# Kernel tuning notes

Measured on AMD Instinct MI355X. Metric: run time of the kernel, lower is better.

The kernel has to match this reference:

```python
import jax, jax.numpy as jnp
import numpy as np

H = 4        # no_heads
CH = 32      # per-head hidden (c_hidden)
INF = 1.0e9

def setup_inputs() -> dict:
    key = jax.random.key(0)
    ks = jax.random.split(key, 8)
    B, I, J, C = 1, 256, 256, 128
    s = 0.02
    return {
        "x": jax.random.normal(ks[0], (B, I, J, C), jnp.float32),
        "mask": jnp.ones((B, I, J), jnp.float32),
        "chunk_size": 0,
        "ln_w": jnp.ones((C,), jnp.float32),
        "ln_b": jnp.zeros((C,), jnp.float32),
        "w_tri": jax.random.normal(ks[1], (C, H), jnp.float32) * s,
        "wq": jax.random.normal(ks[2], (C, H * CH), jnp.float32) * s,
        "wk": jax.random.normal(ks[3], (C, H * CH), jnp.float32) * s,
        "wv": jax.random.normal(ks[4], (C, H * CH), jnp.float32) * s,
        "wg": jax.random.normal(ks[5], (C, H * CH), jnp.float32) * s,
        "bg": jnp.zeros((H * CH,), jnp.float32),
        "wo": jax.random.normal(ks[6], (H * CH, C), jnp.float32) * s,
        "bo": jnp.zeros((C,), jnp.float32),
    }

def _layer_norm(x, w, b, eps=1e-5):
    mu = jnp.mean(x, axis=-1, keepdims=True)
    var = jnp.mean(jnp.square(x - mu), axis=-1, keepdims=True)
    return (x - mu) * jax.lax.rsqrt(var + eps) * w + b

def reference(x, mask, chunk_size, ln_w, ln_b, w_tri, wq, wk, wv, wg, bg, wo, bo):
    # starting=True -> no transpose of (I, J)
    B, I, J, C = x.shape
    xn = _layer_norm(x, ln_w, ln_b)                                   # [B,I,J,C]
    # biases
    mask_bias = (INF * (mask - 1.0))[:, :, None, None, :]             # [B,I,1,1,J]
    tri_bias = jnp.einsum("bijc,ch->bhij", xn, w_tri)[:, None]        # [B,1,H,I,J]
    # gated multi-head attention over the J axis (per row I)
    q = (xn @ wq).reshape(B, I, J, H, CH) * (CH ** -0.5)              # [B,I,J,H,CH]
    k = (xn @ wk).reshape(B, I, J, H, CH)
    v = (xn @ wv).reshape(B, I, J, H, CH)
    scores = jnp.einsum("biqhd,bikhd->bihqk", q, k) + mask_bias + tri_bias
    a = jax.nn.softmax(scores, axis=-1)                               # [B,I,H,J,J]
    o = jnp.einsum("bihqk,bikhd->biqhd", a, v)                        # [B,I,J,H,CH]
    g = jax.nn.sigmoid(xn @ wg + bg).reshape(B, I, J, H, CH)
    o = (o * g).reshape(B, I, J, H * CH)
    return o @ wo + bo                                                # [B,I,J,C]
```

## Files before the change

### kernel.cpp

```cpp
#include <hip/hip_runtime.h>
#include <math.h>

#define NI 256
#define NJ 256
#define NC 128
#define NH 4
#define NCH 32

typedef __attribute__((ext_vector_type(8)))  __bf16        bf16x8;
typedef __attribute__((ext_vector_type(8)))  unsigned short u16x8;
typedef __attribute__((ext_vector_type(4)))  unsigned int   u32x4;
typedef __attribute__((ext_vector_type(16))) float         f32x16;

__device__ __forceinline__ unsigned short f2bf(float f) {
    unsigned u = __builtin_bit_cast(unsigned, f);
    u += 0x7fffu + ((u >> 16) & 1u);
    return (unsigned short)(u >> 16);
}
__device__ __forceinline__ float bf2f(unsigned short s) {
    return __builtin_bit_cast(float, ((unsigned)s) << 16);
}
__device__ __forceinline__ f32x16 fzero16() {
    f32x16 z;
#pragma unroll
    for (int r = 0; r < 16; ++r) z[r] = 0.f;
    return z;
}
__device__ __forceinline__ f32x16 mfma16(bf16x8 a, bf16x8 b, f32x16 c) {
    return __builtin_amdgcn_mfma_f32_32x32x16_bf16(a, b, c, 0, 0, 0);
}

__global__ __launch_bounds__(256) void convert_weights(
    const float* __restrict__ wq, const float* __restrict__ wk,
    const float* __restrict__ wv, const float* __restrict__ wg,
    const float* __restrict__ wo, const float* __restrict__ w_tri,
    unsigned short* __restrict__ Wt_all, unsigned short* __restrict__ Wto,
    unsigned short* __restrict__ Wtri_pad)
{
    int id = blockIdx.x * 256 + threadIdx.x;
    if (id < 4 * 16384) {
        int m = id >> 14, r = id & 16383;
        int kk = r >> 7, c = r & 127;
        const float* W = (m == 0) ? wq : (m == 1) ? wk : (m == 2) ? wv : wg;
        Wt_all[(m * 128 + c) * 128 + kk] = f2bf(W[kk * 128 + c]);
    } else if (id < 5 * 16384) {
        int r = id - 4 * 16384;
        int kk = r >> 7, c = r & 127;
        Wto[c * 128 + kk] = f2bf(wo[kk * 128 + c]);
    } else {
        int r = id - 5 * 16384;
        int col = r >> 7, kk = r & 127;
        Wtri_pad[col * 128 + kk] = (col < NH) ? f2bf(w_tri[kk * NH + col]) : (unsigned short)0;
    }
}

#define XNP 136
__global__ __launch_bounds__(256, 2) void ln_proj_mfma(
    const float* __restrict__ x, const float* __restrict__ ln_w, const float* __restrict__ ln_b,
    const unsigned short* __restrict__ Wt_all, const unsigned short* __restrict__ Wtri_pad,
    const float* __restrict__ bg,
    unsigned short* __restrict__ q, unsigned short* __restrict__ k,
    unsigned short* __restrict__ v, unsigned short* __restrict__ g,
    float* __restrict__ tri)
{
    __shared__ unsigned short xn[64 * XNP];
    const int tid = threadIdx.x;
    const long tok0 = (long)blockIdx.x * 64;

    const int lane8 = tid & 7;
#pragma unroll
    for (int p = 0; p < 2; ++p) {
        const int t = p * 32 + (tid >> 3);
        const float4* xrow = (const float4*)(x + (tok0 + t) * NC + lane8 * 16);
        float4 xv[4];
        float s = 0.f;
#pragma unroll
        for (int u = 0; u < 4; ++u) {
            xv[u] = xrow[u];
            s += xv[u].x + xv[u].y + xv[u].z + xv[u].w;
        }
#pragma unroll
        for (int off = 4; off; off >>= 1) s += __shfl_down(s, off, 8);
        const float mu = __shfl(s, 0, 8) * (1.f / (float)NC);
        float s2 = 0.f;
#pragma unroll
        for (int u = 0; u < 4; ++u) {
            float dx;
            dx = xv[u].x - mu; s2 += dx * dx;
            dx = xv[u].y - mu; s2 += dx * dx;
            dx = xv[u].z - mu; s2 += dx * dx;
            dx = xv[u].w - mu; s2 += dx * dx;
        }
#pragma unroll
        for (int off = 4; off; off >>= 1) s2 += __shfl_down(s2, off, 8);
        const float rstd = rsqrtf(__shfl(s2, 0, 8) * (1.f / (float)NC) + 1e-5f);
#pragma unroll
        for (int u = 0; u < 4; ++u) {
            const int c = lane8 * 16 + u * 4;
            const float4 lw = *(const float4*)(ln_w + c);
            const float4 lb = *(const float4*)(ln_b + c);
            float o0 = (xv[u].x - mu) * rstd * lw.x + lb.x;
            float o1 = (xv[u].y - mu) * rstd * lw.y + lb.y;
            float o2 = (xv[u].z - mu) * rstd * lw.z + lb.z;
            float o3 = (xv[u].w - mu) * rstd * lw.w + lb.w;
            unsigned p0 = (unsigned)f2bf(o0) | ((unsigned)f2bf(o1) << 16);
            unsigned p1 = (unsigned)f2bf(o2) | ((unsigned)f2bf(o3) << 16);
            *(unsigned*)&xn[t * XNP + c]     = p0;
            *(unsigned*)&xn[t * XNP + c + 2] = p1;
        }
    }
    __syncthreads();

    const int w = tid >> 6, L = tid & 63, lh = L >> 5, lc = L & 31;
    f32x16 acc[2][4], accT[2];
#pragma unroll
    for (int mt = 0; mt < 2; ++mt) {
        accT[mt] = fzero16();
#pragma unroll
        for (int nt = 0; nt < 4; ++nt) acc[mt][nt] = fzero16();
    }

#pragma unroll
    for (int k0 = 0; k0 < 8; ++k0) {
        bf16x8 a0 = *(const bf16x8*)&xn[(lc)      * XNP + k0 * 16 + lh * 8];
        bf16x8 a1 = *(const bf16x8*)&xn[(32 + lc) * XNP + k0 * 16 + lh * 8];
#pragma unroll
        for (int nt = 0; nt < 4; ++nt) {
            const int ntile = w + 4 * nt;
            bf16x8 b = *(const bf16x8*)&Wt_all[(ntile * 32 + lc) * 128 + k0 * 16 + lh * 8];
            acc[0][nt] = mfma16(a0, b, acc[0][nt]);
            acc[1][nt] = mfma16(a1, b, acc[1][nt]);
        }
        bf16x8 bt = *(const bf16x8*)&Wtri_pad[lc * 128 + k0 * 16 + lh * 8];
        accT[0] = mfma16(a0, bt, accT[0]);
        accT[1] = mfma16(a1, bt, accT[1]);
    }

    const int a_row = (int)(tok0 >> 8);
    const int b0    = (int)(tok0 & 255);
    int rowl[16];
#pragma unroll
    for (int r = 0; r < 16; ++r) rowl[r] = (r & 3) + 8 * (r >> 2) + 4 * lh;

    const float bgv = bg[w * 32 + lc];
#pragma unroll
    for (int nt = 0; nt < 4; ++nt) {
        unsigned short* O = (nt == 0) ? q : (nt == 1) ? k : (nt == 2) ? v : g;
        unsigned short* Ob = O + (((long)a_row * NH + w) * NJ + b0) * NCH + lc;
#pragma unroll
        for (int mt = 0; mt < 2; ++mt) {
#pragma unroll
            for (int r = 0; r < 16; ++r) {
                const int row = mt * 32 + rowl[r];
                float val = acc[mt][nt][r];
                if (nt == 0) val *= 0.17677669529663689f;
                if (nt == 3) val = __builtin_amdgcn_rcpf(1.f + __expf(-(val + bgv)));
                Ob[(long)row * NCH] = f2bf(val);
            }
        }
    }
    if (lc < NH) {
        float* tb = tri + ((long)lc * NI + a_row) * NJ + b0;
#pragma unroll
        for (int mt = 0; mt < 2; ++mt)
#pragma unroll
            for (int r = 0; r < 16; ++r)
                tb[mt * 32 + rowl[r]] = accT[mt][r];
    }
}

#define LSP 260
__global__ __launch_bounds__(256) void swizzle_triT(
    const float* __restrict__ tri, float* __restrict__ tswz)
{
    __shared__ float Ls[32 * LSP];
    const int h = blockIdx.x, qt = blockIdx.y;
    const int tid = threadIdx.x;
#pragma unroll
    for (int it = 0; it < 8; ++it) {
        const int fi = it * 256 + tid;
        const int row = fi >> 6, c4 = fi & 63;
        *(float4*)&Ls[row * LSP + c4 * 4] =
            *(const float4*)(tri + ((long)h * NI + qt * 32 + row) * NJ + c4 * 4);
    }
    __syncthreads();
    const int kt = tid >> 5;
    const int lane2 = (tid & 31) * 2;
    float* dst = tswz + (((long)(h * 8 + qt) * 8 + kt) * 64 + lane2) * 16;
#pragma unroll
    for (int sub = 0; sub < 2; ++sub) {
        const int lane = lane2 + sub;
        const int lc = lane & 31, lhh = lane >> 5;
        float vals[16];
#pragma unroll
        for (int r = 0; r < 16; ++r)
            vals[r] = Ls[lc * LSP + kt * 32 + (r & 3) + 8 * (r >> 2) + 4 * lhh];
#pragma unroll
        for (int u = 0; u < 4; ++u)
            *(float4*)(dst + sub * 16 + u * 4) =
                make_float4(vals[4*u], vals[4*u+1], vals[4*u+2], vals[4*u+3]);
    }
}

#define KSP 40
#define VTP 264
#define GSP 40
#define OSP 36
__global__ __launch_bounds__(256, 2) void attn_fused(
    const unsigned short* __restrict__ q, const unsigned short* __restrict__ k,
    const unsigned short* __restrict__ v, const unsigned short* __restrict__ g,
    const float* __restrict__ tswz, const float* __restrict__ mask,
    const unsigned short* __restrict__ Wto, const float* __restrict__ bo,
    float* __restrict__ out)
{
    __shared__ char smem[48640];
    unsigned short* Ks = (unsigned short*)smem;
    unsigned short* Vt = (unsigned short*)(smem + 20480);
    unsigned short* Gs = (unsigned short*)(smem + 37376);
    float*       maskb = (float*)(smem + 47616);
    float*        outs = (float*)smem;

    const int i = blockIdx.x, qh = blockIdx.y;
    const int tid = threadIdx.x;
    const int w = tid >> 6, L = tid & 63, lh = L >> 5, lc = L & 31;
    const int qt = qh * 4 + w;
    const int qrow = qt * 32 + lc;

    maskb[tid] = 1.0e9f * (mask[i * NJ + tid] - 1.0f);

    f32x16 outacc[4];
#pragma unroll
    for (int ct = 0; ct < 4; ++ct) outacc[ct] = fzero16();

    for (int h = 0; h < NH; ++h) {
        if (h) __syncthreads();
        const long base = ((long)i * NH + h) * NJ * NCH;

#pragma unroll
        for (int it = 0; it < 4; ++it) {
            const int idx = it * 256 + tid;
            const int key = idx >> 2, c8 = (idx & 3) * 8;
            *(bf16x8*)&Ks[key * KSP + c8] = *(const bf16x8*)(k + base + key * NCH + c8);
        }
        {
            const int key = tid;
            const u16x8 r0 = *(const u16x8*)(v + base + key * NCH);
            const u16x8 r1 = *(const u16x8*)(v + base + key * NCH + 8);
            const u16x8 r2 = *(const u16x8*)(v + base + key * NCH + 16);
            const u16x8 r3 = *(const u16x8*)(v + base + key * NCH + 24);
#pragma unroll
            for (int u = 0; u < 8; ++u) {
                Vt[(u)      * VTP + key] = r0[u];
                Vt[(u + 8)  * VTP + key] = r1[u];
                Vt[(u + 16) * VTP + key] = r2[u];
                Vt[(u + 24) * VTP + key] = r3[u];
            }
        }
#pragma unroll
        for (int it = 0; it < 2; ++it) {
            const int idx = it * 256 + tid;
            const int row = idx >> 2, c8 = (idx & 3) * 8;
            *(bf16x8*)&Gs[row * GSP + c8] =
                *(const bf16x8*)(g + base + (qh * 128 + row) * NCH + c8);
        }
        __syncthreads();

        const bf16x8 a0 = *(const bf16x8*)(q + base + (long)qrow * NCH + lh * 8);
        const bf16x8 a1 = *(const bf16x8*)(q + base + (long)qrow * NCH + 16 + lh * 8);
        const float* tbase = tswz + ((long)(h * 8 + qt) * 8) * 1024 + (long)L * 16;

        float ls = 0.f;
        f32x16 O = fzero16();

#pragma unroll
        for (int t = 0; t < 8; ++t) {
            bf16x8 kb0 = *(const bf16x8*)&Ks[(t * 32 + lc) * KSP + lh * 8];
            bf16x8 kb1 = *(const bf16x8*)&Ks[(t * 32 + lc) * KSP + 16 + lh * 8];
            f32x16 s = fzero16();
            s = mfma16(kb0, a0, s);
            s = mfma16(kb1, a1, s);

            unsigned pk[8];
            const float* tv = tbase + (long)t * 1024;
#pragma unroll
            for (int gg = 0; gg < 4; ++gg) {
                const float4 tb = *(const float4*)(tv + gg * 4);
                const float4 mb = *(const float4*)&maskb[t * 32 + gg * 8 + 4 * lh];
                const float p0 = __expf(fminf(s[4 * gg + 0] + tb.x + mb.x, 30.f));
                const float p1 = __expf(fminf(s[4 * gg + 1] + tb.y + mb.y, 30.f));
                const float p2 = __expf(fminf(s[4 * gg + 2] + tb.z + mb.z, 30.f));
                const float p3 = __expf(fminf(s[4 * gg + 3] + tb.w + mb.w, 30.f));
                ls += (p0 + p1) + (p2 + p3);
                pk[2 * gg]     = (unsigned)f2bf(p0) | ((unsigned)f2bf(p1) << 16);
                pk[2 * gg + 1] = (unsigned)f2bf(p2) | ((unsigned)f2bf(p3) << 16);
            }

#pragma unroll
            for (int ss = 0; ss < 2; ++ss) {
                const unsigned give0 = lh ? pk[4 * ss]     : pk[4 * ss + 2];
                const unsigned give1 = lh ? pk[4 * ss + 1] : pk[4 * ss + 3];
                const unsigned t0 = __shfl_xor(give0, 32);
                const unsigned t1 = __shfl_xor(give1, 32);
                u32x4 bw;
                bw[0] = lh ? t0 : pk[4 * ss];
                bw[1] = lh ? t1 : pk[4 * ss + 1];
                bw[2] = lh ? pk[4 * ss + 2] : t0;
                bw[3] = lh ? pk[4 * ss + 3] : t1;
                const bf16x8 pb = __builtin_bit_cast(bf16x8, bw);
                const bf16x8 va = *(const bf16x8*)&Vt[lc * VTP + t * 32 + ss * 16 + lh * 8];
                O = mfma16(va, pb, O);
            }
        }

        ls += __shfl_xor(ls, 32);
        const float rl = __builtin_amdgcn_rcpf(ls);
        unsigned pk2[8];
#pragma unroll
        for (int gg = 0; gg < 4; ++gg) {
            const ushort4 gv = *(const ushort4*)&Gs[(w * 32 + lc) * GSP + gg * 8 + 4 * lh];
            const float o0 = O[4 * gg + 0] * rl * bf2f(gv.x);
            const float o1 = O[4 * gg + 1] * rl * bf2f(gv.y);
            const float o2 = O[4 * gg + 2] * rl * bf2f(gv.z);
            const float o3 = O[4 * gg + 3] * rl * bf2f(gv.w);
            pk2[2 * gg]     = (unsigned)f2bf(o0) | ((unsigned)f2bf(o1) << 16);
            pk2[2 * gg + 1] = (unsigned)f2bf(o2) | ((unsigned)f2bf(o3) << 16);
        }

#pragma unroll
        for (int ss = 0; ss < 2; ++ss) {
            const unsigned give0 = lh ? pk2[4 * ss]     : pk2[4 * ss + 2];
            const unsigned give1 = lh ? pk2[4 * ss + 1] : pk2[4 * ss + 3];
            const unsigned t0 = __shfl_xor(give0, 32);
            const unsigned t1 = __shfl_xor(give1, 32);
            u32x4 bw;
            bw[0] = lh ? t0 : pk2[4 * ss];
            bw[1] = lh ? t1 : pk2[4 * ss + 1];
            bw[2] = lh ? pk2[4 * ss + 2] : t0;
            bw[3] = lh ? pk2[4 * ss + 3] : t1;
            const bf16x8 ogb = __builtin_bit_cast(bf16x8, bw);
#pragma unroll
            for (int ct = 0; ct < 4; ++ct) {
                const bf16x8 wa = *(const bf16x8*)&Wto[(ct * 32 + lc) * 128 + h * 32 + ss * 16 + lh * 8];
                outacc[ct] = mfma16(wa, ogb, outacc[ct]);
            }
        }
    }

    int rowl[16];
#pragma unroll
    for (int r = 0; r < 16; ++r) rowl[r] = (r & 3) + 8 * (r >> 2) + 4 * lh;
#pragma unroll
    for (int ct = 0; ct < 4; ++ct) {
        __syncthreads();
#pragma unroll
        for (int r = 0; r < 16; ++r)
            outs[(w * 32 + lc) * OSP + rowl[r]] = outacc[ct][r];
        __syncthreads();
#pragma unroll
        for (int it = 0; it < 4; ++it) {
            const int fi = it * 256 + tid;
            const int row = fi >> 3, c4 = fi & 7;
            const float4 vv = *(const float4*)&outs[row * OSP + c4 * 4];
            const float4 bo4 = *(const float4*)(bo + ct * 32 + c4 * 4);
            float4 st;
            st.x = vv.x + bo4.x; st.y = vv.y + bo4.y;
            st.z = vv.z + bo4.z; st.w = vv.w + bo4.w;
            *(float4*)(out + ((long)i * NJ + qh * 128 + row) * NC + ct * 32 + c4 * 4) = st;
        }
    }
}

extern "C" void kernel_launch(void* const* d_in, const int* in_sizes, int n_in,
                              void* d_out, int out_size, void* d_ws, size_t ws_size,
                              hipStream_t stream) {
    const float* x     = (const float*)d_in[0];
    const float* mask  = (const float*)d_in[1];
    const float* ln_w  = (const float*)d_in[3];
    const float* ln_b  = (const float*)d_in[4];
    const float* w_tri = (const float*)d_in[5];
    const float* wq    = (const float*)d_in[6];
    const float* wk    = (const float*)d_in[7];
    const float* wv    = (const float*)d_in[8];
    const float* wg    = (const float*)d_in[9];
    const float* bg    = (const float*)d_in[10];
    const float* wo    = (const float*)d_in[11];
    const float* bo    = (const float*)d_in[12];
    float* out = (float*)d_out;

    char* p = (char*)d_ws;
    const long TOK = (long)NI * NJ;
    const long QB  = TOK * NC * sizeof(unsigned short);
    unsigned short* q  = (unsigned short*)p; p += QB;
    unsigned short* k  = (unsigned short*)p; p += QB;
    unsigned short* v  = (unsigned short*)p; p += QB;
    unsigned short* g  = (unsigned short*)p; p += QB;
    float* tri  = (float*)p; p += (long)NH * NI * NJ * sizeof(float);
    float* tswz = (float*)p; p += (long)NH * NI * NJ * sizeof(float);
    unsigned short* Wt_all   = (unsigned short*)p; p += 4 * 128 * 128 * sizeof(unsigned short);
    unsigned short* Wto      = (unsigned short*)p; p += 128 * 128 * sizeof(unsigned short);
    unsigned short* Wtri_pad = (unsigned short*)p; p += 32 * 128 * sizeof(unsigned short);

    hipLaunchKernelGGL(convert_weights, dim3(336), dim3(256), 0, stream,
                       wq, wk, wv, wg, wo, w_tri, Wt_all, Wto, Wtri_pad);
    hipLaunchKernelGGL(ln_proj_mfma, dim3(TOK / 64), dim3(256), 0, stream,
                       x, ln_w, ln_b, Wt_all, Wtri_pad, bg, q, k, v, g, tri);
    hipLaunchKernelGGL(swizzle_triT, dim3(NH, 8), dim3(256), 0, stream, tri, tswz);
    hipLaunchKernelGGL(attn_fused, dim3(NI, 2), dim3(256), 0, stream,
                       q, k, v, g, tswz, mask, Wto, bo, out);
}
```

Measured before the change: 180.6 us.

## Split attention per head, write swizzled tri bias directly, separate output projection

The projection kernel now writes the triangle bias straight into the swizzled layout the attention kernel reads, which removes the separate swizzle kernel and its extra pass over the tri buffer. The attention kernel is re-gridded to one block per (row, head) with 512 threads, and the head loop is dropped. Instead of fusing the output projection, it writes the gated attention output in bf16 to a workspace buffer. A new outproj kernel then applies Wo and the bias. This raises parallelism and cuts per-block serial work, at the cost of an extra bf16 round trip through global memory and one more launch.

```diff
diff --git a/kernel.cpp b/kernel.cpp
--- a/kernel.cpp
+++ b/kernel.cpp
@@ -61,7 +61,7 @@
     const float* __restrict__ bg,
     unsigned short* __restrict__ q, unsigned short* __restrict__ k,
     unsigned short* __restrict__ v, unsigned short* __restrict__ g,
-    float* __restrict__ tri)
+    float* __restrict__ tswz)
 {
     __shared__ unsigned short xn[64 * XNP];
     const int tid = threadIdx.x;
@@ -160,213 +160,162 @@
         }
     }
     if (lc < NH) {
-        float* tb = tri + ((long)lc * NI + a_row) * NJ + b0;
-#pragma unroll
-        for (int mt = 0; mt < 2; ++mt)
-#pragma unroll
-            for (int r = 0; r < 16; ++r)
-                tb[mt * 32 + rowl[r]] = accT[mt][r];
-    }
-}
-
-#define LSP 260
-__global__ __launch_bounds__(256) void swizzle_triT(
-    const float* __restrict__ tri, float* __restrict__ tswz)
-{
-    __shared__ float Ls[32 * LSP];
-    const int h = blockIdx.x, qt = blockIdx.y;
-    const int tid = threadIdx.x;
-#pragma unroll
-    for (int it = 0; it < 8; ++it) {
-        const int fi = it * 256 + tid;
-        const int row = fi >> 6, c4 = fi & 63;
-        *(float4*)&Ls[row * LSP + c4 * 4] =
-            *(const float4*)(tri + ((long)h * NI + qt * 32 + row) * NJ + c4 * 4);
-    }
-    __syncthreads();
-    const int kt = tid >> 5;
-    const int lane2 = (tid & 31) * 2;
-    float* dst = tswz + (((long)(h * 8 + qt) * 8 + kt) * 64 + lane2) * 16;
-#pragma unroll
-    for (int sub = 0; sub < 2; ++sub) {
-        const int lane = lane2 + sub;
-        const int lc = lane & 31, lhh = lane >> 5;
-        float vals[16];
-#pragma unroll
-        for (int r = 0; r < 16; ++r)
-            vals[r] = Ls[lc * LSP + kt * 32 + (r & 3) + 8 * (r >> 2) + 4 * lhh];
-#pragma unroll
-        for (int u = 0; u < 4; ++u)
-            *(float4*)(dst + sub * 16 + u * 4) =
-                make_float4(vals[4*u], vals[4*u+1], vals[4*u+2], vals[4*u+3]);
+        const int qt_i = a_row >> 5;
+        const int lsw  = ((a_row & 31) + 32 * lh) * 16;
+#pragma unroll
+        for (int mt = 0; mt < 2; ++mt) {
+            float* dst = tswz + ((long)((lc * 8 + qt_i) * 8 + (b0 >> 5) + mt)) * 1024 + lsw;
+#pragma unroll
+            for (int u = 0; u < 4; ++u)
+                *(float4*)(dst + u * 4) = make_float4(accT[mt][4*u],   accT[mt][4*u+1],
+                                                      accT[mt][4*u+2], accT[mt][4*u+3]);
+        }
     }
 }
 
 #define KSP 40
 #define VTP 264
-#define GSP 40
-#define OSP 36
-__global__ __launch_bounds__(256, 2) void attn_fused(
+__global__ __launch_bounds__(512, 4) void attn_fused(
     const unsigned short* __restrict__ q, const unsigned short* __restrict__ k,
     const unsigned short* __restrict__ v, const unsigned short* __restrict__ g,
     const float* __restrict__ tswz, const float* __restrict__ mask,
-    const unsigned short* __restrict__ Wto, const float* __restrict__ bo,
-    float* __restrict__ out)
+    unsigned short* __restrict__ OG)
 {
-    __shared__ char smem[48640];
+    __shared__ char smem[38400];
     unsigned short* Ks = (unsigned short*)smem;
     unsigned short* Vt = (unsigned short*)(smem + 20480);
-    unsigned short* Gs = (unsigned short*)(smem + 37376);
-    float*       maskb = (float*)(smem + 47616);
-    float*        outs = (float*)smem;
-
-    const int i = blockIdx.x, qh = blockIdx.y;
+    float*       maskb = (float*)(smem + 37376);
+
+    const int i = blockIdx.x, h = blockIdx.y;
     const int tid = threadIdx.x;
     const int w = tid >> 6, L = tid & 63, lh = L >> 5, lc = L & 31;
-    const int qt = qh * 4 + w;
+    const int qt = w;
     const int qrow = qt * 32 + lc;
-
-    maskb[tid] = 1.0e9f * (mask[i * NJ + tid] - 1.0f);
-
-    f32x16 outacc[4];
-#pragma unroll
-    for (int ct = 0; ct < 4; ++ct) outacc[ct] = fzero16();
-
-    for (int h = 0; h < NH; ++h) {
-        if (h) __syncthreads();
-        const long base = ((long)i * NH + h) * NJ * NCH;
-
-#pragma unroll
-        for (int it = 0; it < 4; ++it) {
-            const int idx = it * 256 + tid;
-            const int key = idx >> 2, c8 = (idx & 3) * 8;
-            *(bf16x8*)&Ks[key * KSP + c8] = *(const bf16x8*)(k + base + key * NCH + c8);
-        }
-        {
-            const int key = tid;
-            const u16x8 r0 = *(const u16x8*)(v + base + key * NCH);
-            const u16x8 r1 = *(const u16x8*)(v + base + key * NCH + 8);
-            const u16x8 r2 = *(const u16x8*)(v + base + key * NCH + 16);
-            const u16x8 r3 = *(const u16x8*)(v + base + key * NCH + 24);
-#pragma unroll
-            for (int u = 0; u < 8; ++u) {
-                Vt[(u)      * VTP + key] = r0[u];
-                Vt[(u + 8)  * VTP + key] = r1[u];
-                Vt[(u + 16) * VTP + key] = r2[u];
-                Vt[(u + 24) * VTP + key] = r3[u];
-            }
-        }
-#pragma unroll
-        for (int it = 0; it < 2; ++it) {
-            const int idx = it * 256 + tid;
-            const int row = idx >> 2, c8 = (idx & 3) * 8;
-            *(bf16x8*)&Gs[row * GSP + c8] =
-                *(const bf16x8*)(g + base + (qh * 128 + row) * NCH + c8);
-        }
-        __syncthreads();
-
-        const bf16x8 a0 = *(const bf16x8*)(q + base + (long)qrow * NCH + lh * 8);
-        const bf16x8 a1 = *(const bf16x8*)(q + base + (long)qrow * NCH + 16 + lh * 8);
-        const float* tbase = tswz + ((long)(h * 8 + qt) * 8) * 1024 + (long)L * 16;
-
-        float ls = 0.f;
-        f32x16 O = fzero16();
-
-#pragma unroll
-        for (int t = 0; t < 8; ++t) {
-            bf16x8 kb0 = *(const bf16x8*)&Ks[(t * 32 + lc) * KSP + lh * 8];
-            bf16x8 kb1 = *(const bf16x8*)&Ks[(t * 32 + lc) * KSP + 16 + lh * 8];
-            f32x16 s = fzero16();
-            s = mfma16(kb0, a0, s);
-            s = mfma16(kb1, a1, s);
-
-            unsigned pk[8];
-            const float* tv = tbase + (long)t * 1024;
-#pragma unroll
-            for (int gg = 0; gg < 4; ++gg) {
-                const float4 tb = *(const float4*)(tv + gg * 4);
-                const float4 mb = *(const float4*)&maskb[t * 32 + gg * 8 + 4 * lh];
-                const float p0 = __expf(fminf(s[4 * gg + 0] + tb.x + mb.x, 30.f));
-                const float p1 = __expf(fminf(s[4 * gg + 1] + tb.y + mb.y, 30.f));
-                const float p2 = __expf(fminf(s[4 * gg + 2] + tb.z + mb.z, 30.f));
-                const float p3 = __expf(fminf(s[4 * gg + 3] + tb.w + mb.w, 30.f));
-                ls += (p0 + p1) + (p2 + p3);
-                pk[2 * gg]     = (unsigned)f2bf(p0) | ((unsigned)f2bf(p1) << 16);
-                pk[2 * gg + 1] = (unsigned)f2bf(p2) | ((unsigned)f2bf(p3) << 16);
-            }
-
-#pragma unroll
-            for (int ss = 0; ss < 2; ++ss) {
-                const unsigned give0 = lh ? pk[4 * ss]     : pk[4 * ss + 2];
-                const unsigned give1 = lh ? pk[4 * ss + 1] : pk[4 * ss + 3];
-                const unsigned t0 = __shfl_xor(give0, 32);
-                const unsigned t1 = __shfl_xor(give1, 32);
-                u32x4 bw;
-                bw[0] = lh ? t0 : pk[4 * ss];
-                bw[1] = lh ? t1 : pk[4 * ss + 1];
-                bw[2] = lh ? pk[4 * ss + 2] : t0;
-                bw[3] = lh ? pk[4 * ss + 3] : t1;
-                const bf16x8 pb = __builtin_bit_cast(bf16x8, bw);
-                const bf16x8 va = *(const bf16x8*)&Vt[lc * VTP + t * 32 + ss * 16 + lh * 8];
-                O = mfma16(va, pb, O);
-            }
-        }
-
-        ls += __shfl_xor(ls, 32);
-        const float rl = __builtin_amdgcn_rcpf(ls);
-        unsigned pk2[8];
+    const long base = ((long)i * NH + h) * NJ * NCH;
+
+    if (tid < NJ) maskb[tid] = 1.0e9f * (mask[i * NJ + tid] - 1.0f);
+
+#pragma unroll
+    for (int it = 0; it < 2; ++it) {
+        const int idx = it * 512 + tid;
+        const int key = idx >> 2, c8 = (idx & 3) * 8;
+        *(bf16x8*)&Ks[key * KSP + c8] = *(const bf16x8*)(k + base + key * NCH + c8);
+    }
+    {
+        const int key = tid >> 1, c0 = (tid & 1) * 16;
+        const u16x8 r0 = *(const u16x8*)(v + base + key * NCH + c0);
+        const u16x8 r1 = *(const u16x8*)(v + base + key * NCH + c0 + 8);
+#pragma unroll
+        for (int u = 0; u < 8; ++u) {
+            Vt[(c0 + u)     * VTP + key] = r0[u];
+            Vt[(c0 + 8 + u) * VTP + key] = r1[u];
+        }
+    }
+
+    const bf16x8 a0 = *(const bf16x8*)(q + base + (long)qrow * NCH + lh * 8);
+    const bf16x8 a1 = *(const bf16x8*)(q + base + (long)qrow * NCH + 16 + lh * 8);
+    const float* tbase = tswz + ((long)(h * 8 + qt) * 8) * 1024 + (long)L * 16;
+
+    __syncthreads();
+
+    float ls = 0.f;
+    f32x16 O = fzero16();
+
+#pragma unroll
+    for (int t = 0; t < 8; ++t) {
+        bf16x8 kb0 = *(const bf16x8*)&Ks[(t * 32 + lc) * KSP + lh * 8];
+        bf16x8 kb1 = *(const bf16x8*)&Ks[(t * 32 + lc) * KSP + 16 + lh * 8];
+        f32x16 s = fzero16();
+        s = mfma16(kb0, a0, s);
+        s = mfma16(kb1, a1, s);
+
+        unsigned pk[8];
+        const float* tv = tbase + (long)t * 1024;
 #pragma unroll
         for (int gg = 0; gg < 4; ++gg) {
-            const ushort4 gv = *(const ushort4*)&Gs[(w * 32 + lc) * GSP + gg * 8 + 4 * lh];
-            const float o0 = O[4 * gg + 0] * rl * bf2f(gv.x);
-            const float o1 = O[4 * gg + 1] * rl * bf2f(gv.y);
-            const float o2 = O[4 * gg + 2] * rl * bf2f(gv.z);
-            const float o3 = O[4 * gg + 3] * rl * bf2f(gv.w);
-            pk2[2 * gg]     = (unsigned)f2bf(o0) | ((unsigned)f2bf(o1) << 16);
-            pk2[2 * gg + 1] = (unsigned)f2bf(o2) | ((unsigned)f2bf(o3) << 16);
+            const float4 tb = *(const float4*)(tv + gg * 4);
+            const float4 mb = *(const float4*)&maskb[t * 32 + gg * 8 + 4 * lh];
+            const float p0 = __expf(fminf(s[4 * gg + 0] + tb.x + mb.x, 30.f));
+            const float p1 = __expf(fminf(s[4 * gg + 1] + tb.y + mb.y, 30.f));
+            const float p2 = __expf(fminf(s[4 * gg + 2] + tb.z + mb.z, 30.f));
+            const float p3 = __expf(fminf(s[4 * gg + 3] + tb.w + mb.w, 30.f));
+            ls += (p0 + p1) + (p2 + p3);
+            pk[2 * gg]     = (unsigned)f2bf(p0) | ((unsigned)f2bf(p1) << 16);
+            pk[2 * gg + 1] = (unsigned)f2bf(p2) | ((unsigned)f2bf(p3) << 16);
         }
 
 #pragma unroll
         for (int ss = 0; ss < 2; ++ss) {
-            const unsigned give0 = lh ? pk2[4 * ss]     : pk2[4 * ss + 2];
-            const unsigned give1 = lh ? pk2[4 * ss + 1] : pk2[4 * ss + 3];
+            const unsigned give0 = lh ? pk[4 * ss]     : pk[4 * ss + 2];
+            const unsigned give1 = lh ? pk[4 * ss + 1] : pk[4 * ss + 3];
             const unsigned t0 = __shfl_xor(give0, 32);
             const unsigned t1 = __shfl_xor(give1, 32);
             u32x4 bw;
-            bw[0] = lh ? t0 : pk2[4 * ss];
-            bw[1] = lh ? t1 : pk2[4 * ss + 1];
-            bw[2] = lh ? pk2[4 * ss + 2] : t0;
-            bw[3] = lh ? pk2[4 * ss + 3] : t1;
-            const bf16x8 ogb = __builtin_bit_cast(bf16x8, bw);
-#pragma unroll
-            for (int ct = 0; ct < 4; ++ct) {
-                const bf16x8 wa = *(const bf16x8*)&Wto[(ct * 32 + lc) * 128 + h * 32 + ss * 16 + lh * 8];
-                outacc[ct] = mfma16(wa, ogb, outacc[ct]);
-            }
-        }
-    }
-
+            bw[0] = lh ? t0 : pk[4 * ss];
+            bw[1] = lh ? t1 : pk[4 * ss + 1];
+            bw[2] = lh ? pk[4 * ss + 2] : t0;
+            bw[3] = lh ? pk[4 * ss + 3] : t1;
+            const bf16x8 pb = __builtin_bit_cast(bf16x8, bw);
+            const bf16x8 va = *(const bf16x8*)&Vt[lc * VTP + t * 32 + ss * 16 + lh * 8];
+            O = mfma16(va, pb, O);
+        }
+    }
+
+    ls += __shfl_xor(ls, 32);
+    const float rl = __builtin_amdgcn_rcpf(ls);
+    unsigned short* OGrow = OG + (long)(i * NJ + qrow) * NC + h * 32 + 4 * lh;
+#pragma unroll
+    for (int gg = 0; gg < 4; ++gg) {
+        const ushort4 gv = *(const ushort4*)(g + base + (long)qrow * NCH + gg * 8 + 4 * lh);
+        const float o0 = O[4 * gg + 0] * rl * bf2f(gv.x);
+        const float o1 = O[4 * gg + 1] * rl * bf2f(gv.y);
+        const float o2 = O[4 * gg + 2] * rl * bf2f(gv.z);
+        const float o3 = O[4 * gg + 3] * rl * bf2f(gv.w);
+        uint2 st;
+        st.x = (unsigned)f2bf(o0) | ((unsigned)f2bf(o1) << 16);
+        st.y = (unsigned)f2bf(o2) | ((unsigned)f2bf(o3) << 16);
+        *(uint2*)(OGrow + gg * 8) = st;
+    }
+}
+
+#define OGP 136
+__global__ __launch_bounds__(256, 4) void outproj(
+    const unsigned short* __restrict__ OG, const unsigned short* __restrict__ Wto,
+    const float* __restrict__ bo, float* __restrict__ out)
+{
+    __shared__ unsigned short OGs[64 * OGP];
+    const int tid = threadIdx.x;
+    const long tok0 = (long)blockIdx.x * 64;
+#pragma unroll
+    for (int it = 0; it < 4; ++it) {
+        const int idx = it * 256 + tid;
+        const int row = idx >> 4, c8 = (idx & 15) * 8;
+        *(bf16x8*)&OGs[row * OGP + c8] = *(const bf16x8*)(OG + (tok0 + row) * NC + c8);
+    }
+    __syncthreads();
+
+    const int w = tid >> 6, L = tid & 63, lh = L >> 5, lc = L & 31;
+    f32x16 acc[2];
+    acc[0] = fzero16();
+    acc[1] = fzero16();
+#pragma unroll
+    for (int k0 = 0; k0 < 8; ++k0) {
+        const bf16x8 a0 = *(const bf16x8*)&OGs[lc * OGP + k0 * 16 + lh * 8];
+        const bf16x8 a1 = *(const bf16x8*)&OGs[(32 + lc) * OGP + k0 * 16 + lh * 8];
+        const bf16x8 b  = *(const bf16x8*)&Wto[(w * 32 + lc) * 128 + k0 * 16 + lh * 8];
+        acc[0] = mfma16(a0, b, acc[0]);
+        acc[1] = mfma16(a1, b, acc[1]);
+    }
+    const float bov = bo[w * 32 + lc];
     int rowl[16];
 #pragma unroll
     for (int r = 0; r < 16; ++r) rowl[r] = (r & 3) + 8 * (r >> 2) + 4 * lh;
 #pragma unroll
-    for (int ct = 0; ct < 4; ++ct) {
-        __syncthreads();
+    for (int mt = 0; mt < 2; ++mt) {
+        float* Orow = out + (tok0 + mt * 32) * NC + w * 32 + lc;
 #pragma unroll
         for (int r = 0; r < 16; ++r)
-            outs[(w * 32 + lc) * OSP + rowl[r]] = outacc[ct][r];
-        __syncthreads();
-#pragma unroll
-        for (int it = 0; it < 4; ++it) {
-            const int fi = it * 256 + tid;
-            const int row = fi >> 3, c4 = fi & 7;
-            const float4 vv = *(const float4*)&outs[row * OSP + c4 * 4];
-            const float4 bo4 = *(const float4*)(bo + ct * 32 + c4 * 4);
-            float4 st;
-            st.x = vv.x + bo4.x; st.y = vv.y + bo4.y;
-            st.z = vv.z + bo4.z; st.w = vv.w + bo4.w;
-            *(float4*)(out + ((long)i * NJ + qh * 128 + row) * NC + ct * 32 + c4 * 4) = st;
-        }
+            Orow[(long)rowl[r] * NC] = acc[mt][r] + bov;
     }
 }
 
@@ -394,7 +343,7 @@
     unsigned short* k  = (unsigned short*)p; p += QB;
     unsigned short* v  = (unsigned short*)p; p += QB;
     unsigned short* g  = (unsigned short*)p; p += QB;
-    float* tri  = (float*)p; p += (long)NH * NI * NJ * sizeof(float);
+    unsigned short* OG = (unsigned short*)p; p += QB;
     float* tswz = (float*)p; p += (long)NH * NI * NJ * sizeof(float);
     unsigned short* Wt_all   = (unsigned short*)p; p += 4 * 128 * 128 * sizeof(unsigned short);
     unsigned short* Wto      = (unsigned short*)p; p += 128 * 128 * sizeof(unsigned short);
@@ -403,8 +352,9 @@
     hipLaunchKernelGGL(convert_weights, dim3(336), dim3(256), 0, stream,
                        wq, wk, wv, wg, wo, w_tri, Wt_all, Wto, Wtri_pad);
     hipLaunchKernelGGL(ln_proj_mfma, dim3(TOK / 64), dim3(256), 0, stream,
-                       x, ln_w, ln_b, Wt_all, Wtri_pad, bg, q, k, v, g, tri);
-    hipLaunchKernelGGL(swizzle_triT, dim3(NH, 8), dim3(256), 0, stream, tri, tswz);
-    hipLaunchKernelGGL(attn_fused, dim3(NI, 2), dim3(256), 0, stream,
-                       q, k, v, g, tswz, mask, Wto, bo, out);
-}
+                       x, ln_w, ln_b, Wt_all, Wtri_pad, bg, q, k, v, g, tswz);
+    hipLaunchKernelGGL(attn_fused, dim3(NI, NH), dim3(512), 0, stream,
+                       q, k, v, g, tswz, mask, OG);
+    hipLaunchKernelGGL(outproj, dim3(TOK / 64), dim3(256), 0, stream,
+                       OG, Wto, bo, out);
+}
```

New measurement: 226.7 us. 25.5% more time.

## Write triangle bias in swizzled layout directly and stage QKVG stores through LDS

Applied to the files above, without the earlier changes.

The projection kernel now writes the triangle-bias tile straight into the MFMA-swizzled layout the attention kernel reads. This removes the separate swizzle kernel launch and the intermediate fp32 tri buffer. The q/k/v/g epilogue also stages each output tile in the existing LDS xn buffer and then writes 16-byte vectorized rows, replacing scattered 2-byte global stores. The cost is extra __syncthreads and LDS traffic in the epilogue.

```diff
diff --git a/kernel.cpp b/kernel.cpp
--- a/kernel.cpp
+++ b/kernel.cpp
@@ -6,6 +6,7 @@
 #define NC 128
 #define NH 4
 #define NCH 32
+#define TOKS ((long)NI * NJ)
 
 typedef __attribute__((ext_vector_type(8)))  __bf16        bf16x8;
 typedef __attribute__((ext_vector_type(8)))  unsigned short u16x8;
@@ -61,7 +62,7 @@
     const float* __restrict__ bg,
     unsigned short* __restrict__ q, unsigned short* __restrict__ k,
     unsigned short* __restrict__ v, unsigned short* __restrict__ g,
-    float* __restrict__ tri)
+    float* __restrict__ tswz)
 {
     __shared__ unsigned short xn[64 * XNP];
     const int tid = threadIdx.x;
@@ -142,11 +143,24 @@
 #pragma unroll
     for (int r = 0; r < 16; ++r) rowl[r] = (r & 3) + 8 * (r >> 2) + 4 * lh;
 
+    if (lc < NH) {
+        const int qt_i = a_row >> 5;
+        const int lsw  = ((a_row & 31) + 32 * lh) * 16;
+#pragma unroll
+        for (int mt = 0; mt < 2; ++mt) {
+            float* dst = tswz + ((long)((lc * 8 + qt_i) * 8 + (b0 >> 5) + mt)) * 1024 + lsw;
+#pragma unroll
+            for (int u = 0; u < 4; ++u)
+                *(float4*)(dst + u * 4) = make_float4(accT[mt][4*u],   accT[mt][4*u+1],
+                                                      accT[mt][4*u+2], accT[mt][4*u+3]);
+        }
+    }
+
     const float bgv = bg[w * 32 + lc];
 #pragma unroll
     for (int nt = 0; nt < 4; ++nt) {
         unsigned short* O = (nt == 0) ? q : (nt == 1) ? k : (nt == 2) ? v : g;
-        unsigned short* Ob = O + (((long)a_row * NH + w) * NJ + b0) * NCH + lc;
+        __syncthreads();
 #pragma unroll
         for (int mt = 0; mt < 2; ++mt) {
 #pragma unroll
@@ -155,50 +169,16 @@
                 float val = acc[mt][nt][r];
                 if (nt == 0) val *= 0.17677669529663689f;
                 if (nt == 3) val = __builtin_amdgcn_rcpf(1.f + __expf(-(val + bgv)));
-                Ob[(long)row * NCH] = f2bf(val);
-            }
-        }
-    }
-    if (lc < NH) {
-        float* tb = tri + ((long)lc * NI + a_row) * NJ + b0;
-#pragma unroll
-        for (int mt = 0; mt < 2; ++mt)
-#pragma unroll
-            for (int r = 0; r < 16; ++r)
-                tb[mt * 32 + rowl[r]] = accT[mt][r];
-    }
-}
-
-#define LSP 260
-__global__ __launch_bounds__(256) void swizzle_triT(
-    const float* __restrict__ tri, float* __restrict__ tswz)
-{
-    __shared__ float Ls[32 * LSP];
-    const int h = blockIdx.x, qt = blockIdx.y;
-    const int tid = threadIdx.x;
-#pragma unroll
-    for (int it = 0; it < 8; ++it) {
-        const int fi = it * 256 + tid;
-        const int row = fi >> 6, c4 = fi & 63;
-        *(float4*)&Ls[row * LSP + c4 * 4] =
-            *(const float4*)(tri + ((long)h * NI + qt * 32 + row) * NJ + c4 * 4);
-    }
-    __syncthreads();
-    const int kt = tid >> 5;
-    const int lane2 = (tid & 31) * 2;
-    float* dst = tswz + (((long)(h * 8 + qt) * 8 + kt) * 64 + lane2) * 16;
-#pragma unroll
-    for (int sub = 0; sub < 2; ++sub) {
-        const int lane = lane2 + sub;
-        const int lc = lane & 31, lhh = lane >> 5;
-        float vals[16];
-#pragma unroll
-        for (int r = 0; r < 16; ++r)
-            vals[r] = Ls[lc * LSP + kt * 32 + (r & 3) + 8 * (r >> 2) + 4 * lhh];
-#pragma unroll
-        for (int u = 0; u < 4; ++u)
-            *(float4*)(dst + sub * 16 + u * 4) =
-                make_float4(vals[4*u], vals[4*u+1], vals[4*u+2], vals[4*u+3]);
+                xn[row * XNP + w * 32 + lc] = f2bf(val);
+            }
+        }
+        __syncthreads();
+#pragma unroll
+        for (int it = 0; it < 4; ++it) {
+            const int row = tid >> 2, cc = (tid & 3) * 8;
+            *(u16x8*)(O + (((long)a_row * NH + it) * NJ + b0 + row) * NCH + cc) =
+                *(const u16x8*)&xn[row * XNP + it * 32 + cc];
+        }
     }
 }
 
@@ -388,13 +368,11 @@
     float* out = (float*)d_out;
 
     char* p = (char*)d_ws;
-    const long TOK = (long)NI * NJ;
-    const long QB  = TOK * NC * sizeof(unsigned short);
+    const long QB  = TOKS * NC * sizeof(unsigned short);
     unsigned short* q  = (unsigned short*)p; p += QB;
     unsigned short* k  = (unsigned short*)p; p += QB;
     unsigned short* v  = (unsigned short*)p; p += QB;
     unsigned short* g  = (unsigned short*)p; p += QB;
-    float* tri  = (float*)p; p += (long)NH * NI * NJ * sizeof(float);
     float* tswz = (float*)p; p += (long)NH * NI * NJ * sizeof(float);
     unsigned short* Wt_all   = (unsigned short*)p; p += 4 * 128 * 128 * sizeof(unsigned short);
     unsigned short* Wto      = (unsigned short*)p; p += 128 * 128 * sizeof(unsigned short);
@@ -402,9 +380,8 @@
 
     hipLaunchKernelGGL(convert_weights, dim3(336), dim3(256), 0, stream,
                        wq, wk, wv, wg, wo, w_tri, Wt_all, Wto, Wtri_pad);
-    hipLaunchKernelGGL(ln_proj_mfma, dim3(TOK / 64), dim3(256), 0, stream,
-                       x, ln_w, ln_b, Wt_all, Wtri_pad, bg, q, k, v, g, tri);
-    hipLaunchKernelGGL(swizzle_triT, dim3(NH, 8), dim3(256), 0, stream, tri, tswz);
+    hipLaunchKernelGGL(ln_proj_mfma, dim3(TOKS / 64), dim3(256), 0, stream,
+                       x, ln_w, ln_b, Wt_all, Wtri_pad, bg, q, k, v, g, tswz);
     hipLaunchKernelGGL(attn_fused, dim3(NI, 2), dim3(256), 0, stream,
                        q, k, v, g, tswz, mask, Wto, bo, out);
 }
```

Result: no change. 177.4 us (-1.8%).
